# Optimization experiments

Measured on AMD Instinct MI355X. Metric: run time of the kernel, lower is better.

The kernel has to match this reference:

```python
import jax, jax.numpy as jnp
import numpy as np

D_MODEL = 1024
NUM_HEADS = 16
HEAD_DIM = D_MODEL // NUM_HEADS


def setup_inputs() -> dict:
    key = jax.random.key(0)
    k_x, k_wq, k_wo = jax.random.split(key, 3)
    x = jax.random.normal(k_x, (2, 2048, D_MODEL), dtype=jnp.float32)
    # Xavier-uniform init to mirror _reset_parameters
    lim_qkv = float(np.sqrt(6.0 / (D_MODEL + 3 * D_MODEL)))
    lim_o = float(np.sqrt(6.0 / (D_MODEL + D_MODEL)))
    w_qkv = jax.random.uniform(k_wq, (3 * D_MODEL, D_MODEL), jnp.float32, -lim_qkv, lim_qkv)
    b_qkv = jnp.zeros((3 * D_MODEL,), jnp.float32)
    w_o = jax.random.uniform(k_wo, (D_MODEL, D_MODEL), jnp.float32, -lim_o, lim_o)
    b_o = jnp.zeros((D_MODEL,), jnp.float32)
    return {"x": x, "w_qkv": w_qkv, "b_qkv": b_qkv, "w_o": w_o, "b_o": b_o}


def reference(x, w_qkv, b_qkv, w_o, b_o):
    B, T, C = x.shape
    H, Dh = NUM_HEADS, HEAD_DIM
    # Fused QKV projection: [B,T,3C]
    qkv = jnp.einsum('btc,oc->bto', x, w_qkv) + b_qkv
    qkv = qkv.reshape(B, T, 3, H, Dh)
    q = qkv[:, :, 0].transpose(0, 2, 1, 3)  # [B,H,T,Dh]
    k = qkv[:, :, 1].transpose(0, 2, 1, 3)
    v = qkv[:, :, 2].transpose(0, 2, 1, 3)
    scale = 1.0 / jnp.sqrt(jnp.asarray(Dh, x.dtype))
    scores = jnp.einsum('bhqd,bhkd->bhqk', q, k) * scale  # [B,H,T,T]
    attn = jax.nn.softmax(scores, axis=-1)
    out = jnp.einsum('bhqk,bhkd->bhqd', attn, v)  # [B,H,T,Dh]
    out = out.transpose(0, 2, 1, 3).reshape(B, T, C)
    return jnp.einsum('btc,oc->bto', out, w_o) + b_o
```

## Files before the change

### kernel.cpp

```cpp
#include <hip/hip_runtime.h>
#include <math.h>

#define SEQ   2048
#define BATCH 2
#define CDIM  1024
#define NH    16
#define DH    64
#define BH    (BATCH*NH)
#define KVB   64
#define QBLK  128

#define QSCALE 0.18033688011112042f
#define SMSHIFT 12.0f

typedef __attribute__((ext_vector_type(8))) short bf16x8;
typedef __attribute__((ext_vector_type(4))) short s16x4;
typedef __attribute__((ext_vector_type(4))) float f32x4;
typedef __attribute__((ext_vector_type(2))) unsigned u32x2;

__device__ __forceinline__ short f2bf(float f) {
  union { float f; unsigned u; } v; v.f = f;
  unsigned r = (v.u + 0x7FFFu + ((v.u >> 16) & 1u)) >> 16;
  return (short)r;
}
__device__ __forceinline__ float bf2f(short s) {
  union { unsigned u; float f; } v; v.u = ((unsigned)(unsigned short)s) << 16;
  return v.f;
}
__device__ __forceinline__ float fexp2(float x) {
  float r; asm("v_exp_f32 %0, %1" : "=v"(r) : "v"(x)); return r;
}
__device__ __forceinline__ unsigned cvtpk_bf16(float a, float b) {
  unsigned r; asm("v_cvt_pk_bf16_f32 %0, %1, %2" : "=v"(r) : "v"(a), "v"(b));
  return r;
}
__device__ __forceinline__ void gload_lds16(const void* g, void* l) {
  __builtin_amdgcn_global_load_lds(
      (const __attribute__((address_space(1))) void*)g,
      (__attribute__((address_space(3))) void*)l, 16, 0, 0);
}

template<int R>
__device__ __forceinline__ void stage_tile(const short* __restrict__ g,
                                           short* __restrict__ lds, int tid) {
#pragma unroll
  for (int rd = 0; rd < R / 64; ++rd) {
    const int idx = rd * 256 + tid;
    const int row = idx >> 2, ch = idx & 3;
    const int sch = ch ^ ((row >> 1) & 3);
    gload_lds16(&g[(long)row * CDIM + sch * 8], &lds[idx * 8]);
  }
}
__device__ __forceinline__ bf16x8 frag(const short* __restrict__ lds,
                                       int row, int g) {
  const int sch = g ^ ((row >> 1) & 3);
  return *(const bf16x8*)&lds[row * 32 + sch * 8];
}

__device__ __forceinline__ int aswz(int row, int ch) {
  return (row << 6) + ((ch ^ (row & 7)) << 3);
}

__global__ __launch_bounds__(256)
void cvt_hilo(const float* __restrict__ in, short* __restrict__ hi,
              short* __restrict__ lo, int n4) {
  const int i = blockIdx.x * 256 + threadIdx.x;
  if (i >= n4) return;
  const float4 v = reinterpret_cast<const float4*>(in)[i];
  s16x4 h, l;
  h[0] = f2bf(v.x); h[1] = f2bf(v.y); h[2] = f2bf(v.z); h[3] = f2bf(v.w);
  l[0] = f2bf(v.x - bf2f(h[0]));
  l[1] = f2bf(v.y - bf2f(h[1]));
  l[2] = f2bf(v.z - bf2f(h[2]));
  l[3] = f2bf(v.w - bf2f(h[3]));
  reinterpret_cast<s16x4*>(hi)[i] = h;
  reinterpret_cast<s16x4*>(lo)[i] = l;
}

__global__ __launch_bounds__(256)
void qkv_mfma(const short* __restrict__ xh, const short* __restrict__ xl,
              const short* __restrict__ wh, const short* __restrict__ wl,
              const float* __restrict__ bias,
              short* __restrict__ qh, short* __restrict__ ql,
              short* __restrict__ kh, short* __restrict__ kl,
              short* __restrict__ vt) {
  __shared__ short S[2][4][128 * 32];
  const int tid  = threadIdx.x;
  const int wave = tid >> 6, lane = tid & 63;
  const int l15  = lane & 15, g = lane >> 4;
  const int wr   = wave >> 1, wc = wave & 1;
  const int m0   = blockIdx.y * 128, n0 = blockIdx.x * 128;

  const short* Abh = xh + (long)m0 * CDIM;
  const short* Abl = xl + (long)m0 * CDIM;
  const short* Bbh = wh + (long)n0 * CDIM;
  const short* Bbl = wl + (long)n0 * CDIM;

  f32x4 acc[4][4];
#pragma unroll
  for (int mi = 0; mi < 4; ++mi)
#pragma unroll
    for (int ni = 0; ni < 4; ++ni) {
      acc[mi][ni][0] = 0.f; acc[mi][ni][1] = 0.f;
      acc[mi][ni][2] = 0.f; acc[mi][ni][3] = 0.f;
    }

  stage_tile<128>(Abh, S[0][0], tid);
  stage_tile<128>(Abl, S[0][1], tid);
  stage_tile<128>(Bbh, S[0][2], tid);
  stage_tile<128>(Bbl, S[0][3], tid);
  __syncthreads();

  for (int k = 0; k < CDIM / 32; ++k) {
    const int cur = k & 1;
    if (k < CDIM / 32 - 1) {
      const int k1 = (k + 1) * 32;
      stage_tile<128>(Abh + k1, S[cur ^ 1][0], tid);
      stage_tile<128>(Abl + k1, S[cur ^ 1][1], tid);
      stage_tile<128>(Bbh + k1, S[cur ^ 1][2], tid);
      stage_tile<128>(Bbl + k1, S[cur ^ 1][3], tid);
    }
    bf16x8 ah[4], al2[4], bh2[4], bl2[4];
#pragma unroll
    for (int mi = 0; mi < 4; ++mi) {
      const int r = wr * 64 + mi * 16 + l15;
      ah[mi]  = frag(S[cur][0], r, g);
      al2[mi] = frag(S[cur][1], r, g);
    }
#pragma unroll
    for (int ni = 0; ni < 4; ++ni) {
      const int r = wc * 64 + ni * 16 + l15;
      bh2[ni] = frag(S[cur][2], r, g);
      bl2[ni] = frag(S[cur][3], r, g);
    }
#pragma unroll
    for (int mi = 0; mi < 4; ++mi)
#pragma unroll
      for (int ni = 0; ni < 4; ++ni) {
        acc[mi][ni] = __builtin_amdgcn_mfma_f32_16x16x32_bf16(
            ah[mi], bh2[ni], acc[mi][ni], 0, 0, 0);
        acc[mi][ni] = __builtin_amdgcn_mfma_f32_16x16x32_bf16(
            al2[mi], bh2[ni], acc[mi][ni], 0, 0, 0);
        acc[mi][ni] = __builtin_amdgcn_mfma_f32_16x16x32_bf16(
            ah[mi], bl2[ni], acc[mi][ni], 0, 0, 0);
      }
    __syncthreads();
  }

  const int s = n0 >> 10;
  const int hbase = (n0 & 1023) >> 6;
  if (s < 2) {
    short* hb = (s == 0) ? qh : kh;
    short* lb = (s == 0) ? ql : kl;
    const float sc = (s == 0) ? QSCALE : 1.0f;
    float bv[4];
#pragma unroll
    for (int ni = 0; ni < 4; ++ni) bv[ni] = bias[n0 + wc * 64 + ni * 16 + l15];
    short* T = &S[0][0][0];
#pragma unroll
    for (int p = 0; p < 2; ++p) {
#pragma unroll
      for (int mi = 0; mi < 4; ++mi)
#pragma unroll
        for (int ni = 0; ni < 4; ++ni)
#pragma unroll
          for (int r = 0; r < 4; ++r) {
            const int row = wr * 64 + mi * 16 + g * 4 + r;
            const int col = wc * 64 + ni * 16 + l15;
            const float v = (acc[mi][ni][r] + bv[ni]) * sc;
            const short hv = f2bf(v);
            T[row * 136 + col] = (p == 0) ? hv : f2bf(v - bf2f(hv));
          }
      __syncthreads();
      short* dst = (p == 0) ? hb : lb;
#pragma unroll
      for (int it = 0; it < 8; ++it) {
        const int idx = it * 256 + tid;
        const int row = idx >> 4, c16 = idx & 15;
        const bf16x8 vv = *(const bf16x8*)&T[row * 136 + c16 * 8];
        const int h = hbase + (c16 >> 3), dh0 = (c16 & 7) * 8;
        const int t = m0 + row, bi = t >> 11, tt = t & 2047;
        *(bf16x8*)&dst[(((long)(bi * NH + h)) * SEQ + tt) * DH + dh0] = vv;
      }
      __syncthreads();
    }
  } else {
#pragma unroll
    for (int ni = 0; ni < 4; ++ni) {
      const int n_g = n0 + wc * 64 + ni * 16 + l15;
      const int o = n_g & 1023, h = o >> 6, dh = o & 63;
      const float bvv = bias[n_g];
#pragma unroll
      for (int mi = 0; mi < 4; ++mi) {
        const int mr = m0 + wr * 64 + mi * 16 + g * 4;
        const int bi = mr >> 11, t = mr & 2047;
        s16x4 pv;
#pragma unroll
        for (int r = 0; r < 4; ++r) pv[r] = f2bf(acc[mi][ni][r] + bvv);
        *(s16x4*)&vt[(((long)(bi * NH + h)) * DH + dh) * SEQ + t] = pv;
      }
    }
  }
}

__global__ __launch_bounds__(256)
void fattn_mfma(const short* __restrict__ qhg, const short* __restrict__ qlg,
                const short* __restrict__ khg, const short* __restrict__ klg,
                const short* __restrict__ vtg,
                short* __restrict__ abh, short* __restrict__ abl) {
  __shared__ short Khs[2][KVB * 64];
  __shared__ short Kls[2][KVB * 64];
  __shared__ short Vts[2][DH * 64];
  __shared__ short Ps[QBLK * 64];

  const int tid  = threadIdx.x;
  const int wave = tid >> 6;
  const int lane = tid & 63;
  const int l15  = lane & 15;
  const int g    = lane >> 4;
  const int bh   = blockIdx.x;
  const int q0   = blockIdx.y * QBLK;
  const int qw   = q0 + wave * 32;

  bf16x8 Qh[2][2], Ql[2][2];
#pragma unroll
  for (int qt = 0; qt < 2; ++qt) {
    const long qrow = ((long)bh * SEQ + qw + qt * 16 + l15) * DH;
#pragma unroll
    for (int c = 0; c < 2; ++c) {
      Qh[qt][c] = *(const bf16x8*)&qhg[qrow + c * 32 + g * 8];
      Ql[qt][c] = *(const bf16x8*)&qlg[qrow + c * 32 + g * 8];
    }
  }

  f32x4 o[2][4];
#pragma unroll
  for (int qt = 0; qt < 2; ++qt)
#pragma unroll
    for (int d = 0; d < 4; ++d) {
      o[qt][d][0] = 0.f; o[qt][d][1] = 0.f;
      o[qt][d][2] = 0.f; o[qt][d][3] = 0.f;
    }
  float lrun[2] = {0.f, 0.f};

  long ksrc[2], vsrc[2];
  int ldst[2];
#pragma unroll
  for (int it = 0; it < 2; ++it) {
    const int idx = it * 256 + tid;
    const int srow = idx >> 3;
    const int gch = (idx & 7) ^ (srow & 7);
    ksrc[it] = (long)bh * SEQ * DH + (long)srow * DH + gch * 8;
    vsrc[it] = ((long)bh * DH + srow) * SEQ + gch * 8;
    ldst[it] = idx * 8;
  }

#pragma unroll
  for (int it = 0; it < 2; ++it) {
    gload_lds16(&khg[ksrc[it]], &Khs[0][ldst[it]]);
    gload_lds16(&klg[ksrc[it]], &Kls[0][ldst[it]]);
    gload_lds16(&vtg[vsrc[it]], &Vts[0][ldst[it]]);
  }
  __syncthreads();

  int cur = 0;
  for (int kt = 0; kt < SEQ / KVB; ++kt) {
    if (kt + 1 < SEQ / KVB) {
#pragma unroll
      for (int it = 0; it < 2; ++it) {
        const long ko = ksrc[it] + (long)(kt + 1) * (KVB * DH);
        gload_lds16(&khg[ko], &Khs[cur ^ 1][ldst[it]]);
        gload_lds16(&klg[ko], &Kls[cur ^ 1][ldst[it]]);
        gload_lds16(&vtg[vsrc[it] + (kt + 1) * KVB], &Vts[cur ^ 1][ldst[it]]);
      }
    }

    const short* Kc = Khs[cur];
    const short* Lc = Kls[cur];
    f32x4 s[2][4];
    __builtin_amdgcn_s_setprio(1);
#pragma unroll
    for (int kc = 0; kc < 4; ++kc) {
      const int a0 = aswz(kc * 16 + l15, g);
      const int a1 = aswz(kc * 16 + l15, 4 + g);
      const bf16x8 kb0 = *(const bf16x8*)&Kc[a0];
      const bf16x8 lb0 = *(const bf16x8*)&Lc[a0];
      const bf16x8 kb1 = *(const bf16x8*)&Kc[a1];
      const bf16x8 lb1 = *(const bf16x8*)&Lc[a1];
#pragma unroll
      for (int qt = 0; qt < 2; ++qt) {
        f32x4 a; a[0] = 0.f; a[1] = 0.f; a[2] = 0.f; a[3] = 0.f;
        a = __builtin_amdgcn_mfma_f32_16x16x32_bf16(kb0, Qh[qt][0], a, 0, 0, 0);
        a = __builtin_amdgcn_mfma_f32_16x16x32_bf16(kb0, Ql[qt][0], a, 0, 0, 0);
        a = __builtin_amdgcn_mfma_f32_16x16x32_bf16(lb0, Qh[qt][0], a, 0, 0, 0);
        a = __builtin_amdgcn_mfma_f32_16x16x32_bf16(kb1, Qh[qt][1], a, 0, 0, 0);
        a = __builtin_amdgcn_mfma_f32_16x16x32_bf16(kb1, Ql[qt][1], a, 0, 0, 0);
        a = __builtin_amdgcn_mfma_f32_16x16x32_bf16(lb1, Qh[qt][1], a, 0, 0, 0);
        s[qt][kc] = a;
      }
    }
    __builtin_amdgcn_s_setprio(0);

#pragma unroll
    for (int qt = 0; qt < 2; ++qt) {
      const int row = wave * 32 + qt * 16 + l15;
#pragma unroll
      for (int kc = 0; kc < 4; ++kc) {
        const float p0 = fexp2(s[qt][kc][0] - SMSHIFT);
        const float p1 = fexp2(s[qt][kc][1] - SMSHIFT);
        const float p2 = fexp2(s[qt][kc][2] - SMSHIFT);
        const float p3 = fexp2(s[qt][kc][3] - SMSHIFT);
        lrun[qt] += (p0 + p1) + (p2 + p3);
        u32x2 w; w[0] = cvtpk_bf16(p0, p1); w[1] = cvtpk_bf16(p2, p3);
        const int ch = (2 * kc + (g >> 1)) ^ (row & 7);
        *(u32x2*)&Ps[(row << 6) + ch * 8 + (g & 1) * 4] = w;
      }
    }

    const short* Vc = Vts[cur];
    __builtin_amdgcn_s_setprio(1);
#pragma unroll
    for (int kk = 0; kk < 2; ++kk) {
      bf16x8 vf[4];
#pragma unroll
      for (int d = 0; d < 4; ++d)
        vf[d] = *(const bf16x8*)&Vc[aswz(d * 16 + l15, kk * 4 + g)];
#pragma unroll
      for (int qt = 0; qt < 2; ++qt) {
        const bf16x8 pa =
            *(const bf16x8*)&Ps[aswz(wave * 32 + qt * 16 + l15, kk * 4 + g)];
#pragma unroll
        for (int d = 0; d < 4; ++d)
          o[qt][d] = __builtin_amdgcn_mfma_f32_16x16x32_bf16(
              pa, vf[d], o[qt][d], 0, 0, 0);
      }
    }
    __builtin_amdgcn_s_setprio(0);

    __syncthreads();
    cur ^= 1;
  }

  const int b = bh >> 4, hh = bh & 15;
#pragma unroll
  for (int qt = 0; qt < 2; ++qt) {
    float rs = lrun[qt];
    rs += __shfl_xor(rs, 16);
    rs += __shfl_xor(rs, 32);
#pragma unroll
    for (int r = 0; r < 4; ++r) {
      const float lv = __shfl(rs, 16 * g + 4 * g + r);
      const float inv = 1.0f / lv;
      const int t = qw + qt * 16 + 4 * g + r;
      const long base = ((long)(b * SEQ + t)) * CDIM + hh * DH + l15;
#pragma unroll
      for (int d = 0; d < 4; ++d) {
        const float v = o[qt][d][r] * inv;
        const short hv = f2bf(v);
        abh[base + d * 16] = hv;
        abl[base + d * 16] = f2bf(v - bf2f(hv));
      }
    }
  }
}

__global__ __launch_bounds__(256)
void out_mfma(const short* __restrict__ ah, const short* __restrict__ al,
              const short* __restrict__ wh, const short* __restrict__ wl,
              const float* __restrict__ bias, float* __restrict__ out) {
  __shared__ short S[2][12288];
  const int tid  = threadIdx.x;
  const int wave = tid >> 6, lane = tid & 63;
  const int l15  = lane & 15, g = lane >> 4;
  const int wr   = wave >> 1, wc = wave & 1;
  const int m0   = blockIdx.y * 128, n0 = blockIdx.x * 64;

  const short* Abh = ah + (long)m0 * CDIM;
  const short* Abl = al + (long)m0 * CDIM;
  const short* Bbh = wh + (long)n0 * CDIM;
  const short* Bbl = wl + (long)n0 * CDIM;

  f32x4 acc[4][2];
#pragma unroll
  for (int mi = 0; mi < 4; ++mi)
#pragma unroll
    for (int ni = 0; ni < 2; ++ni) {
      acc[mi][ni][0] = 0.f; acc[mi][ni][1] = 0.f;
      acc[mi][ni][2] = 0.f; acc[mi][ni][3] = 0.f;
    }

  stage_tile<128>(Abh, &S[0][0], tid);
  stage_tile<128>(Abl, &S[0][4096], tid);
  stage_tile<64>(Bbh, &S[0][8192], tid);
  stage_tile<64>(Bbl, &S[0][10240], tid);
  __syncthreads();

  for (int k = 0; k < CDIM / 32; ++k) {
    const int cur = k & 1;
    if (k < CDIM / 32 - 1) {
      const int k1 = (k + 1) * 32;
      stage_tile<128>(Abh + k1, &S[cur ^ 1][0], tid);
      stage_tile<128>(Abl + k1, &S[cur ^ 1][4096], tid);
      stage_tile<64>(Bbh + k1, &S[cur ^ 1][8192], tid);
      stage_tile<64>(Bbl + k1, &S[cur ^ 1][10240], tid);
    }
    bf16x8 af[4], af2[4], bf1[2], bf2[2];
#pragma unroll
    for (int mi = 0; mi < 4; ++mi) {
      const int r = wr * 64 + mi * 16 + l15;
      af[mi]  = frag(&S[cur][0], r, g);
      af2[mi] = frag(&S[cur][4096], r, g);
    }
#pragma unroll
    for (int ni = 0; ni < 2; ++ni) {
      const int r = wc * 32 + ni * 16 + l15;
      bf1[ni] = frag(&S[cur][8192], r, g);
      bf2[ni] = frag(&S[cur][10240], r, g);
    }
#pragma unroll
    for (int mi = 0; mi < 4; ++mi)
#pragma unroll
      for (int ni = 0; ni < 2; ++ni) {
        acc[mi][ni] = __builtin_amdgcn_mfma_f32_16x16x32_bf16(
            af[mi], bf1[ni], acc[mi][ni], 0, 0, 0);
        acc[mi][ni] = __builtin_amdgcn_mfma_f32_16x16x32_bf16(
            af2[mi], bf1[ni], acc[mi][ni], 0, 0, 0);
        acc[mi][ni] = __builtin_amdgcn_mfma_f32_16x16x32_bf16(
            af[mi], bf2[ni], acc[mi][ni], 0, 0, 0);
      }
    __syncthreads();
  }

#pragma unroll
  for (int ni = 0; ni < 2; ++ni) {
    const int n = n0 + wc * 32 + ni * 16 + l15;
    const float bv = bias[n];
#pragma unroll
    for (int mi = 0; mi < 4; ++mi) {
#pragma unroll
      for (int r = 0; r < 4; ++r) {
        const int m = m0 + wr * 64 + mi * 16 + g * 4 + r;
        out[(long)m * CDIM + n] = acc[mi][ni][r] + bv;
      }
    }
  }
}

__global__ __launch_bounds__(256)
void qkv_gemm_f32(const float* __restrict__ x, const float* __restrict__ w,
                  const float* __restrict__ bias,
                  short* __restrict__ qh, short* __restrict__ ql,
                  short* __restrict__ kh, short* __restrict__ kl,
                  short* __restrict__ vt) {
  __shared__ float As[16][65];
  __shared__ float Bs[16][65];
  const int tid = threadIdx.x;
  const int tx = tid & 15, ty = tid >> 4;
  const int m0 = blockIdx.y * 64;
  const int n0 = blockIdx.x * 64;
  const int lr = tid >> 2;
  const int lc = (tid & 3) << 2;
  float acc[4][4] = {};
  const float* ap = x + (long)(m0 + lr) * CDIM + lc;
  const float* bp = w + (long)(n0 + lr) * CDIM + lc;
  for (int k0 = 0; k0 < CDIM; k0 += 16) {
    float4 av = *reinterpret_cast<const float4*>(ap + k0);
    float4 bv = *reinterpret_cast<const float4*>(bp + k0);
    __syncthreads();
    As[lc + 0][lr] = av.x; As[lc + 1][lr] = av.y;
    As[lc + 2][lr] = av.z; As[lc + 3][lr] = av.w;
    Bs[lc + 0][lr] = bv.x; Bs[lc + 1][lr] = bv.y;
    Bs[lc + 2][lr] = bv.z; Bs[lc + 3][lr] = bv.w;
    __syncthreads();
#pragma unroll
    for (int kk = 0; kk < 16; ++kk) {
      float a[4], bb[4];
#pragma unroll
      for (int i = 0; i < 4; ++i) a[i] = As[kk][ty * 4 + i];
#pragma unroll
      for (int j = 0; j < 4; ++j) bb[j] = Bs[kk][tx * 4 + j];
#pragma unroll
      for (int i = 0; i < 4; ++i)
#pragma unroll
        for (int j = 0; j < 4; ++j)
          acc[i][j] = fmaf(a[i], bb[j], acc[i][j]);
    }
  }
  const int s = n0 >> 10;
  const int hh = (n0 & 1023) >> 6;
  const float4 bq = *reinterpret_cast<const float4*>(&bias[n0 + tx * 4]);
  if (s < 2) {
    const float scale = (s == 0) ? QSCALE : 1.0f;
    short* hb = (s == 0) ? qh : kh;
    short* lb = (s == 0) ? ql : kl;
#pragma unroll
    for (int i = 0; i < 4; ++i) {
      const int m = m0 + ty * 4 + i;
      const int bi = m >> 11, t = m & 2047;
      float v0 = (acc[i][0] + bq.x) * scale;
      float v1 = (acc[i][1] + bq.y) * scale;
      float v2 = (acc[i][2] + bq.z) * scale;
      float v3 = (acc[i][3] + bq.w) * scale;
      s16x4 hv, lv;
      hv[0] = f2bf(v0); hv[1] = f2bf(v1); hv[2] = f2bf(v2); hv[3] = f2bf(v3);
      lv[0] = f2bf(v0 - bf2f(hv[0]));
      lv[1] = f2bf(v1 - bf2f(hv[1]));
      lv[2] = f2bf(v2 - bf2f(hv[2]));
      lv[3] = f2bf(v3 - bf2f(hv[3]));
      const long base = (((long)(bi * NH + hh)) * SEQ + t) * DH + tx * 4;
      *(s16x4*)&hb[base] = hv;
      *(s16x4*)&lb[base] = lv;
    }
  } else {
#pragma unroll
    for (int i = 0; i < 4; ++i) {
      const int m = m0 + ty * 4 + i;
      const int bi = m >> 11, t = m & 2047;
      float vv[4] = {acc[i][0] + bq.x, acc[i][1] + bq.y,
                     acc[i][2] + bq.z, acc[i][3] + bq.w};
#pragma unroll
      for (int j = 0; j < 4; ++j)
        vt[((long)(bi * NH + hh) * DH + tx * 4 + j) * SEQ + t] = f2bf(vv[j]);
    }
  }
}

__global__ __launch_bounds__(256)
void out_gemm_f32(const short* __restrict__ ah, const short* __restrict__ al,
                  const float* __restrict__ w,
                  const float* __restrict__ bias, float* __restrict__ out) {
  __shared__ float As[16][65];
  __shared__ float Bs[16][65];
  const int tid = threadIdx.x;
  const int tx = tid & 15, ty = tid >> 4;
  const int m0 = blockIdx.y * 64;
  const int n0 = blockIdx.x * 64;
  const int lr = tid >> 2;
  const int lc = (tid & 3) << 2;
  float acc[4][4] = {};
  const long arow = (long)(m0 + lr) * CDIM + lc;
  const float* bp = w + (long)(n0 + lr) * CDIM + lc;
  for (int k0 = 0; k0 < CDIM; k0 += 16) {
    s16x4 hv = *(const s16x4*)&ah[arow + k0];
    s16x4 lv = *(const s16x4*)&al[arow + k0];
    float4 bv = *reinterpret_cast<const float4*>(bp + k0);
    __syncthreads();
#pragma unroll
    for (int j = 0; j < 4; ++j) As[lc + j][lr] = bf2f(hv[j]) + bf2f(lv[j]);
    Bs[lc + 0][lr] = bv.x; Bs[lc + 1][lr] = bv.y;
    Bs[lc + 2][lr] = bv.z; Bs[lc + 3][lr] = bv.w;
    __syncthreads();
#pragma unroll
    for (int kk = 0; kk < 16; ++kk) {
      float av2[4], bb[4];
#pragma unroll
      for (int i = 0; i < 4; ++i) av2[i] = As[kk][ty * 4 + i];
#pragma unroll
      for (int j = 0; j < 4; ++j) bb[j] = Bs[kk][tx * 4 + j];
#pragma unroll
      for (int i = 0; i < 4; ++i)
#pragma unroll
        for (int j = 0; j < 4; ++j)
          acc[i][j] = fmaf(av2[i], bb[j], acc[i][j]);
    }
  }
  const float4 bq = *reinterpret_cast<const float4*>(&bias[n0 + tx * 4]);
#pragma unroll
  for (int i = 0; i < 4; ++i) {
    const int m = m0 + ty * 4 + i;
    float4 v;
    v.x = acc[i][0] + bq.x; v.y = acc[i][1] + bq.y;
    v.z = acc[i][2] + bq.z; v.w = acc[i][3] + bq.w;
    *reinterpret_cast<float4*>(&out[(long)m * CDIM + n0 + tx * 4]) = v;
  }
}

extern "C" void kernel_launch(void* const* d_in, const int* in_sizes, int n_in,
                              void* d_out, int out_size, void* d_ws, size_t ws_size,
                              hipStream_t stream) {
  (void)in_sizes; (void)n_in; (void)out_size;
  const float* x     = (const float*)d_in[0];
  const float* w_qkv = (const float*)d_in[1];
  const float* b_qkv = (const float*)d_in[2];
  const float* w_o   = (const float*)d_in[3];
  const float* b_o   = (const float*)d_in[4];
  float* out = (float*)d_out;

  const size_t NEED = 71303168;
  if (ws_size >= NEED) {
    short* base = (short*)d_ws;
    short* xh  = base;
    short* xl  = base + 4194304;
    short* wqh = base + 8388608;
    short* wql = base + 11534336;
    short* qh  = base + 14680064;
    short* ql  = base + 18874368;
    short* kh  = base + 23068672;
    short* kl  = base + 27262976;
    short* vt  = base + 31457280;
    short* woh = wqh;
    short* wol = wqh + 1048576;
    short* abh = xh;
    short* abl = xl;

    cvt_hilo<<<4096, 256, 0, stream>>>(x, xh, xl, 1048576);
    cvt_hilo<<<3072, 256, 0, stream>>>(w_qkv, wqh, wql, 786432);
    qkv_mfma<<<dim3(24, 32), 256, 0, stream>>>(xh, xl, wqh, wql, b_qkv,
                                               qh, ql, kh, kl, vt);
    cvt_hilo<<<1024, 256, 0, stream>>>(w_o, woh, wol, 262144);
    fattn_mfma<<<dim3(BH, SEQ / QBLK), 256, 0, stream>>>(qh, ql, kh, kl, vt,
                                                         abh, abl);
    out_mfma<<<dim3(16, 32), 256, 0, stream>>>(abh, abl, woh, wol, b_o, out);
  } else {
    short* qh  = (short*)d_ws;
    short* ql  = qh + 4194304;
    short* kh  = ql + 4194304;
    short* kl  = kh + 4194304;
    short* vt  = kl + 4194304;
    short* abh = vt + 4194304;
    short* abl = abh + 4194304;

    qkv_gemm_f32<<<dim3(48, 64), 256, 0, stream>>>(x, w_qkv, b_qkv,
                                                   qh, ql, kh, kl, vt);
    fattn_mfma<<<dim3(BH, SEQ / QBLK), 256, 0, stream>>>(qh, ql, kh, kl, vt,
                                                         abh, abl);
    out_gemm_f32<<<dim3(16, 64), 256, 0, stream>>>(abh, abl, w_o, b_o, out);
  }
}
```

Baseline: 227.0 us.

## Remap QKV and attention workgroups per XCD, single-buffer QKV LDS, merge conversions

Blocks in the QKV GEMM and the attention kernel are remapped from a 2D grid to a 1D grid. Consecutive workgroups on the same XCD now share the same rows or heads, which is meant to improve L2 reuse. The QKV GEMM drops LDS double buffering in favour of a single buffer, adds a launch-bounds occupancy hint of 4 blocks, and interleaves B fragment loads with the MFMAs to cut register pressure. The x and w_qkv hi/lo conversions are merged into one launch to save launch overhead. The single-buffered loop now waits on each tile load with no prefetch overlap, and relies on higher occupancy to hide that latency.

```diff
diff --git a/kernel.cpp b/kernel.cpp
--- a/kernel.cpp
+++ b/kernel.cpp
@@ -59,6 +59,26 @@
 
 __device__ __forceinline__ int aswz(int row, int ch) {
   return (row << 6) + ((ch ^ (row & 7)) << 3);
+}
+
+__global__ __launch_bounds__(256)
+void cvt_hilo2(const float* __restrict__ a, short* __restrict__ ah,
+               short* __restrict__ al, int na4,
+               const float* __restrict__ b, short* __restrict__ bh,
+               short* __restrict__ bl, int nb4) {
+  int i = blockIdx.x * 256 + threadIdx.x;
+  const float* src; short *dh, *dl;
+  if (i < na4) { src = a; dh = ah; dl = al; }
+  else { i -= na4; if (i >= nb4) return; src = b; dh = bh; dl = bl; }
+  const float4 v = reinterpret_cast<const float4*>(src)[i];
+  s16x4 h, l;
+  h[0] = f2bf(v.x); h[1] = f2bf(v.y); h[2] = f2bf(v.z); h[3] = f2bf(v.w);
+  l[0] = f2bf(v.x - bf2f(h[0]));
+  l[1] = f2bf(v.y - bf2f(h[1]));
+  l[2] = f2bf(v.z - bf2f(h[2]));
+  l[3] = f2bf(v.w - bf2f(h[3]));
+  reinterpret_cast<s16x4*>(dh)[i] = h;
+  reinterpret_cast<s16x4*>(dl)[i] = l;
 }
 
 __global__ __launch_bounds__(256)
@@ -77,19 +97,27 @@
   reinterpret_cast<s16x4*>(lo)[i] = l;
 }
 
-__global__ __launch_bounds__(256)
+__global__ __launch_bounds__(256, 4)
 void qkv_mfma(const short* __restrict__ xh, const short* __restrict__ xl,
               const short* __restrict__ wh, const short* __restrict__ wl,
               const float* __restrict__ bias,
               short* __restrict__ qh, short* __restrict__ ql,
               short* __restrict__ kh, short* __restrict__ kl,
               short* __restrict__ vt) {
-  __shared__ short S[2][4][128 * 32];
+  __shared__ short S[17408];
+  short* Ah_s = S;
+  short* Al_s = S + 4096;
+  short* Bh_s = S + 8192;
+  short* Bl_s = S + 12288;
+
   const int tid  = threadIdx.x;
   const int wave = tid >> 6, lane = tid & 63;
   const int l15  = lane & 15, g = lane >> 4;
   const int wr   = wave >> 1, wc = wave & 1;
-  const int m0   = blockIdx.y * 128, n0 = blockIdx.x * 128;
+  const int wgid = blockIdx.x;
+  const int xcd  = wgid & 7, pos = wgid >> 3;
+  const int m0   = (xcd * 4 + pos / 24) * 128;
+  const int n0   = (pos % 24) * 128;
 
   const short* Abh = xh + (long)m0 * CDIM;
   const short* Abl = xl + (long)m0 * CDIM;
@@ -105,45 +133,34 @@
       acc[mi][ni][2] = 0.f; acc[mi][ni][3] = 0.f;
     }
 
-  stage_tile<128>(Abh, S[0][0], tid);
-  stage_tile<128>(Abl, S[0][1], tid);
-  stage_tile<128>(Bbh, S[0][2], tid);
-  stage_tile<128>(Bbl, S[0][3], tid);
-  __syncthreads();
-
-  for (int k = 0; k < CDIM / 32; ++k) {
-    const int cur = k & 1;
-    if (k < CDIM / 32 - 1) {
-      const int k1 = (k + 1) * 32;
-      stage_tile<128>(Abh + k1, S[cur ^ 1][0], tid);
-      stage_tile<128>(Abl + k1, S[cur ^ 1][1], tid);
-      stage_tile<128>(Bbh + k1, S[cur ^ 1][2], tid);
-      stage_tile<128>(Bbl + k1, S[cur ^ 1][3], tid);
-    }
-    bf16x8 ah[4], al2[4], bh2[4], bl2[4];
+  for (int k0 = 0; k0 < CDIM; k0 += 32) {
+    stage_tile<128>(Abh + k0, Ah_s, tid);
+    stage_tile<128>(Abl + k0, Al_s, tid);
+    stage_tile<128>(Bbh + k0, Bh_s, tid);
+    stage_tile<128>(Bbl + k0, Bl_s, tid);
+    __syncthreads();
+    bf16x8 a_h[4], a_l[4];
 #pragma unroll
     for (int mi = 0; mi < 4; ++mi) {
       const int r = wr * 64 + mi * 16 + l15;
-      ah[mi]  = frag(S[cur][0], r, g);
-      al2[mi] = frag(S[cur][1], r, g);
+      a_h[mi] = frag(Ah_s, r, g);
+      a_l[mi] = frag(Al_s, r, g);
     }
 #pragma unroll
     for (int ni = 0; ni < 4; ++ni) {
       const int r = wc * 64 + ni * 16 + l15;
-      bh2[ni] = frag(S[cur][2], r, g);
-      bl2[ni] = frag(S[cur][3], r, g);
-    }
-#pragma unroll
-    for (int mi = 0; mi < 4; ++mi)
-#pragma unroll
-      for (int ni = 0; ni < 4; ++ni) {
+      const bf16x8 b_h = frag(Bh_s, r, g);
+      const bf16x8 b_l = frag(Bl_s, r, g);
+#pragma unroll
+      for (int mi = 0; mi < 4; ++mi) {
         acc[mi][ni] = __builtin_amdgcn_mfma_f32_16x16x32_bf16(
-            ah[mi], bh2[ni], acc[mi][ni], 0, 0, 0);
+            a_h[mi], b_h, acc[mi][ni], 0, 0, 0);
         acc[mi][ni] = __builtin_amdgcn_mfma_f32_16x16x32_bf16(
-            al2[mi], bh2[ni], acc[mi][ni], 0, 0, 0);
+            a_l[mi], b_h, acc[mi][ni], 0, 0, 0);
         acc[mi][ni] = __builtin_amdgcn_mfma_f32_16x16x32_bf16(
-            ah[mi], bl2[ni], acc[mi][ni], 0, 0, 0);
-      }
+            a_h[mi], b_l, acc[mi][ni], 0, 0, 0);
+      }
+    }
     __syncthreads();
   }
 
@@ -156,7 +173,7 @@
     float bv[4];
 #pragma unroll
     for (int ni = 0; ni < 4; ++ni) bv[ni] = bias[n0 + wc * 64 + ni * 16 + l15];
-    short* T = &S[0][0][0];
+    short* T = S;
 #pragma unroll
     for (int p = 0; p < 2; ++p) {
 #pragma unroll
@@ -218,8 +235,10 @@
   const int lane = tid & 63;
   const int l15  = lane & 15;
   const int g    = lane >> 4;
-  const int bh   = blockIdx.x;
-  const int q0   = blockIdx.y * QBLK;
+  const int wgid = blockIdx.x;
+  const int xcd  = wgid & 7, pos = wgid >> 3;
+  const int bh   = xcd * 4 + (pos >> 4);
+  const int q0   = (pos & 15) * QBLK;
   const int qw   = q0 + wave * 32;
 
   bf16x8 Qh[2][2], Ql[2][2];
@@ -603,13 +622,12 @@
     short* abh = xh;
     short* abl = xl;
 
-    cvt_hilo<<<4096, 256, 0, stream>>>(x, xh, xl, 1048576);
-    cvt_hilo<<<3072, 256, 0, stream>>>(w_qkv, wqh, wql, 786432);
-    qkv_mfma<<<dim3(24, 32), 256, 0, stream>>>(xh, xl, wqh, wql, b_qkv,
-                                               qh, ql, kh, kl, vt);
+    cvt_hilo2<<<7168, 256, 0, stream>>>(x, xh, xl, 1048576,
+                                        w_qkv, wqh, wql, 786432);
+    qkv_mfma<<<768, 256, 0, stream>>>(xh, xl, wqh, wql, b_qkv,
+                                      qh, ql, kh, kl, vt);
     cvt_hilo<<<1024, 256, 0, stream>>>(w_o, woh, wol, 262144);
-    fattn_mfma<<<dim3(BH, SEQ / QBLK), 256, 0, stream>>>(qh, ql, kh, kl, vt,
-                                                         abh, abl);
+    fattn_mfma<<<512, 256, 0, stream>>>(qh, ql, kh, kl, vt, abh, abl);
     out_mfma<<<dim3(16, 32), 256, 0, stream>>>(abh, abl, woh, wol, b_o, out);
   } else {
     short* qh  = (short*)d_ws;
@@ -622,8 +640,7 @@
 
     qkv_gemm_f32<<<dim3(48, 64), 256, 0, stream>>>(x, w_qkv, b_qkv,
                                                    qh, ql, kh, kl, vt);
-    fattn_mfma<<<dim3(BH, SEQ / QBLK), 256, 0, stream>>>(qh, ql, kh, kl, vt,
-                                                         abh, abl);
+    fattn_mfma<<<512, 256, 0, stream>>>(qh, ql, kh, kl, vt, abh, abl);
     out_gemm_f32<<<dim3(16, 64), 256, 0, stream>>>(abh, abl, w_o, b_o, out);
   }
 }
```

After: 215.3 us. 5.1% less time.

## Remap workgroups per XCD, fuse conversion launches, and pipeline QKV GEMM waits

Applied to the files above, without the earlier changes.

Workgroup IDs in the QKV GEMM and attention kernels are remapped so that blocks sharing the same rows or head land on the same XCD, which is meant to improve L2 reuse. The two fp32-to-bf16 hi/lo conversion launches are merged into one kernel. In the QKV GEMM main loop, __syncthreads is replaced by explicit vmcnt waits and raw barriers, and the MFMA section runs at raised wave priority so the next tile's loads overlap with compute. The explicit vmcnt(8) count depends on how many loads each stage issues, which makes the code fragile if the staging changes.

```diff
diff --git a/kernel.cpp b/kernel.cpp
--- a/kernel.cpp
+++ b/kernel.cpp
@@ -59,6 +59,26 @@
 
 __device__ __forceinline__ int aswz(int row, int ch) {
   return (row << 6) + ((ch ^ (row & 7)) << 3);
+}
+
+__global__ __launch_bounds__(256)
+void cvt_hilo2(const float* __restrict__ a, short* __restrict__ ah,
+               short* __restrict__ al, int na4,
+               const float* __restrict__ b, short* __restrict__ bh,
+               short* __restrict__ bl, int nb4) {
+  int i = blockIdx.x * 256 + threadIdx.x;
+  const float* src; short *dh, *dl;
+  if (i < na4) { src = a; dh = ah; dl = al; }
+  else { i -= na4; if (i >= nb4) return; src = b; dh = bh; dl = bl; }
+  const float4 v = reinterpret_cast<const float4*>(src)[i];
+  s16x4 h, l;
+  h[0] = f2bf(v.x); h[1] = f2bf(v.y); h[2] = f2bf(v.z); h[3] = f2bf(v.w);
+  l[0] = f2bf(v.x - bf2f(h[0]));
+  l[1] = f2bf(v.y - bf2f(h[1]));
+  l[2] = f2bf(v.z - bf2f(h[2]));
+  l[3] = f2bf(v.w - bf2f(h[3]));
+  reinterpret_cast<s16x4*>(dh)[i] = h;
+  reinterpret_cast<s16x4*>(dl)[i] = l;
 }
 
 __global__ __launch_bounds__(256)
@@ -89,7 +109,10 @@
   const int wave = tid >> 6, lane = tid & 63;
   const int l15  = lane & 15, g = lane >> 4;
   const int wr   = wave >> 1, wc = wave & 1;
-  const int m0   = blockIdx.y * 128, n0 = blockIdx.x * 128;
+  const int wgid = blockIdx.x;
+  const int xcd  = wgid & 7, pos = wgid >> 3;
+  const int m0   = (xcd * 4 + pos / 24) * 128;
+  const int n0   = (pos % 24) * 128;
 
   const short* Abh = xh + (long)m0 * CDIM;
   const short* Abl = xl + (long)m0 * CDIM;
@@ -109,7 +132,6 @@
   stage_tile<128>(Abl, S[0][1], tid);
   stage_tile<128>(Bbh, S[0][2], tid);
   stage_tile<128>(Bbl, S[0][3], tid);
-  __syncthreads();
 
   for (int k = 0; k < CDIM / 32; ++k) {
     const int cur = k & 1;
@@ -119,7 +141,14 @@
       stage_tile<128>(Abl + k1, S[cur ^ 1][1], tid);
       stage_tile<128>(Bbh + k1, S[cur ^ 1][2], tid);
       stage_tile<128>(Bbl + k1, S[cur ^ 1][3], tid);
-    }
+      asm volatile("s_waitcnt vmcnt(8)" ::: "memory");
+    } else {
+      asm volatile("s_waitcnt vmcnt(0)" ::: "memory");
+    }
+    __builtin_amdgcn_sched_barrier(0);
+    __builtin_amdgcn_s_barrier();
+    __builtin_amdgcn_sched_barrier(0);
+
     bf16x8 ah[4], al2[4], bh2[4], bl2[4];
 #pragma unroll
     for (int mi = 0; mi < 4; ++mi) {
@@ -133,6 +162,7 @@
       bh2[ni] = frag(S[cur][2], r, g);
       bl2[ni] = frag(S[cur][3], r, g);
     }
+    __builtin_amdgcn_s_setprio(1);
 #pragma unroll
     for (int mi = 0; mi < 4; ++mi)
 #pragma unroll
@@ -144,7 +174,11 @@
         acc[mi][ni] = __builtin_amdgcn_mfma_f32_16x16x32_bf16(
             ah[mi], bl2[ni], acc[mi][ni], 0, 0, 0);
       }
-    __syncthreads();
+    __builtin_amdgcn_s_setprio(0);
+
+    __builtin_amdgcn_sched_barrier(0);
+    __builtin_amdgcn_s_barrier();
+    __builtin_amdgcn_sched_barrier(0);
   }
 
   const int s = n0 >> 10;
@@ -218,8 +252,10 @@
   const int lane = tid & 63;
   const int l15  = lane & 15;
   const int g    = lane >> 4;
-  const int bh   = blockIdx.x;
-  const int q0   = blockIdx.y * QBLK;
+  const int wgid = blockIdx.x;
+  const int xcd  = wgid & 7, pos = wgid >> 3;
+  const int bh   = xcd * 4 + (pos >> 4);
+  const int q0   = (pos & 15) * QBLK;
   const int qw   = q0 + wave * 32;
 
   bf16x8 Qh[2][2], Ql[2][2];
@@ -603,13 +639,12 @@
     short* abh = xh;
     short* abl = xl;
 
-    cvt_hilo<<<4096, 256, 0, stream>>>(x, xh, xl, 1048576);
-    cvt_hilo<<<3072, 256, 0, stream>>>(w_qkv, wqh, wql, 786432);
-    qkv_mfma<<<dim3(24, 32), 256, 0, stream>>>(xh, xl, wqh, wql, b_qkv,
-                                               qh, ql, kh, kl, vt);
+    cvt_hilo2<<<7168, 256, 0, stream>>>(x, xh, xl, 1048576,
+                                        w_qkv, wqh, wql, 786432);
+    qkv_mfma<<<768, 256, 0, stream>>>(xh, xl, wqh, wql, b_qkv,
+                                      qh, ql, kh, kl, vt);
     cvt_hilo<<<1024, 256, 0, stream>>>(w_o, woh, wol, 262144);
-    fattn_mfma<<<dim3(BH, SEQ / QBLK), 256, 0, stream>>>(qh, ql, kh, kl, vt,
-                                                         abh, abl);
+    fattn_mfma<<<512, 256, 0, stream>>>(qh, ql, kh, kl, vt, abh, abl);
     out_mfma<<<dim3(16, 32), 256, 0, stream>>>(abh, abl, woh, wol, b_o, out);
   } else {
     short* qh  = (short*)d_ws;
@@ -622,8 +657,7 @@
 
     qkv_gemm_f32<<<dim3(48, 64), 256, 0, stream>>>(x, w_qkv, b_qkv,
                                                    qh, ql, kh, kl, vt);
-    fattn_mfma<<<dim3(BH, SEQ / QBLK), 256, 0, stream>>>(qh, ql, kh, kl, vt,
-                                                         abh, abl);
+    fattn_mfma<<<512, 256, 0, stream>>>(qh, ql, kh, kl, vt, abh, abl);
     out_gemm_f32<<<dim3(16, 64), 256, 0, stream>>>(abh, abl, w_o, b_o, out);
   }
 }
```

New measurement: 207.2 us. 8.7% less time.
